# Kernel optimization log

Measured on AMD Instinct MI355X. Metric: run time of the kernel, lower is better.

## Reference

```python
import jax, jax.numpy as jnp
import numpy as np

B = 64            # batch
C = 2             # num_channels (BSF syndrome: X and Z)
L = 64            # lattice size
N = 16            # gradient (histogram) size
BIN = 360 // N    # bin_size = 22 degrees
EPS = 1e-5        # BatchNorm2d default eps


def setup_inputs() -> dict:
    key = jax.random.key(0)
    k1, = jax.random.split(key, 1)
    # syndrome in BSF: binary 0/1 values (torch.nonzero picks the set bits)
    x = jax.random.randint(k1, (B, C * L * L * L), 0, 2).astype(jnp.float32)
    gamma = jnp.ones((C,), jnp.float32)   # BatchNorm2d weight
    beta = jnp.zeros((C,), jnp.float32)   # BatchNorm2d bias
    return {"x": x, "gamma": gamma, "beta": beta}


def _bin_tables():
    # Per lattice site (i,j,k): magnitude and flattened (ax, az) bin index.
    c = jnp.arange(L, dtype=jnp.float32)
    i = c[:, None, None]
    j = c[None, :, None]
    k = c[None, None, :]
    mag = jnp.sqrt(i * i + j * j + k * k)          # (L,L,L)
    x_comp = jnp.sqrt(j * j + k * k)
    z_comp = jnp.sqrt(j * j + i * i)
    deg = 180.0 / jnp.pi
    # atan2 results are in [0, pi] here, so int() truncation == floor
    ax = jnp.floor(jnp.arctan2(x_comp, i) * deg / BIN).astype(jnp.int32)
    az = jnp.floor(jnp.arctan2(k, z_comp) * deg / BIN).astype(jnp.int32)
    bins = (ax * N + az).reshape(-1)               # (L^3,) flattened (ax,az)
    return mag.reshape(-1), bins


def reference(x, gamma, beta):
    mag, bins = _bin_tables()
    # torch.nonzero + indexed update == mask-weighted scatter of magnitudes.
    # x is 0/1, so x * mag equals the mags of the nonzero sites (0 elsewhere).
    xw = x.reshape(B, C, L * L * L) * mag                     # (B,C,L^3)
    g = jnp.zeros((B, C, N * N), x.dtype).at[:, :, bins].add(xw)
    g = g.reshape(B, C, N, N)
    # BatchNorm2d, training mode: per-channel batch statistics (biased var)
    mean = g.mean(axis=(0, 2, 3), keepdims=True)
    var = ((g - mean) ** 2).mean(axis=(0, 2, 3), keepdims=True)
    gn = (g - mean) * jax.lax.rsqrt(var + EPS)
    return gn * gamma[None, :, None, None] + beta[None, :, None, None]
```

## Files before the change

### kernel.cpp

```cpp
#include <hip/hip_runtime.h>


#define BINS_PAD 80
#define SLOTS 10

__global__ __launch_bounds__(256)
void bin_table_kernel(unsigned char* __restrict__ tab,
                      float* __restrict__ g,
                      float* __restrict__ mag) {
    int v = blockIdx.x * 256 + threadIdx.x;
    int i = v >> 12, j = (v >> 6) & 63, k = v & 63;
    double xc2 = (double)(j * j + k * k);
    double zc2 = (double)(i * i + j * j);
    double i2  = (double)(i * i);
    double k2  = (double)(k * k);
    const double T1 = 0.4040262258351568  * 0.4040262258351568;
    const double T2 = 0.9656887748070740  * 0.9656887748070740;
    const double T3 = 2.2460367739042161  * 2.2460367739042161;
    const double T4 = 28.636253282915602  * 28.636253282915602;
    int ax = (xc2 > i2 * T1) + (xc2 > i2 * T2) + (xc2 > i2 * T3) + (xc2 > i2 * T4);
    int az = (k2 > zc2 * T1) + (k2 > zc2 * T2) + (k2 > zc2 * T3) + (k2 > zc2 * T4);
    tab[v] = (unsigned char)(ax * 16 + az);
    float kf  = (float)k;
    float r2f = (float)(i * i + j * j);
    mag[v] = sqrtf(fmaf(kf, kf, r2f));
    if (v < 32768) g[v] = 0.0f;
}

__global__ __launch_bounds__(256)
void scatter_kernel(const float4* __restrict__ x4,
                    const uint4* __restrict__ tab4,
                    const float4* __restrict__ mag4,
                    float* __restrict__ g) {
    __shared__ unsigned long long slot[256][SLOTS];
    __shared__ float hist[BINS_PAD];
    int tid = threadIdx.x;
    int p   = blockIdx.x >> 6;
    int i   = blockIdx.x & 63;

    const unsigned long long SENT = ((unsigned long long)69u) << 32;
    #pragma unroll
    for (int s = 0; s < SLOTS; ++s) slot[tid][s] = SENT;
    if (tid < BINS_PAD) hist[tid] = 0.0f;

    const float4* xs = x4 + (size_t)p * 65536 + (size_t)i * 1024 + 4 * (size_t)tid;
    const float4* ms = mag4 + (size_t)i * 1024 + 4 * (size_t)tid;
    uint4  tb  = tab4[i * 256 + tid];
    float4 xq0 = xs[0], xq1 = xs[1], xq2 = xs[2], xq3 = xs[3];
    float4 mq0 = ms[0], mq1 = ms[1], mq2 = ms[2], mq3 = ms[3];

    float4       xq[4] = {xq0, xq1, xq2, xq3};
    float4       mq[4] = {mq0, mq1, mq2, mq3};
    unsigned int uq[4] = {tb.x, tb.y, tb.z, tb.w};

    int          prev = -1;
    unsigned int off  = (unsigned int)-8;
    float        acc  = 0.0f;
    char* myslot = (char*)slot[tid];

    #pragma unroll
    for (int q = 0; q < 4; ++q) {
        unsigned int u = uq[q];
        #pragma unroll
        for (int e = 0; e < 4; ++e) {
            float xe = (e == 0) ? xq[q].x : (e == 1) ? xq[q].y : (e == 2) ? xq[q].z : xq[q].w;
            float me = (e == 0) ? mq[q].x : (e == 1) ? mq[q].y : (e == 2) ? mq[q].z : mq[q].w;
            float val = xe * me;
            int   b   = (u >> (8 * e)) & 255;
            bool  ch  = (b != prev);
            off += ch ? 8u : 0u;
            acc  = ch ? val : (acc + val);
            prev = b;
            *(unsigned long long*)(myslot + off) =
                (((unsigned long long)(unsigned)b) << 32)
              | (unsigned long long)__float_as_uint(acc);
        }
    }
    __syncthreads();

    unsigned long long* mys = slot[tid];
    #pragma unroll
    for (int s = 0; s < SLOTS; ++s) {
        unsigned long long pk = mys[s];
        float av = __uint_as_float((unsigned int)pk);
        if (av != 0.0f) {
            unsigned int bb = (unsigned int)(pk >> 32);
            atomicAdd(&hist[bb], av);
        }
    }
    __syncthreads();

    if (tid < BINS_PAD) {
        float hv = hist[tid];
        if (hv != 0.0f) atomicAdd(&g[p * 256 + tid], hv);
    }
}

__global__ __launch_bounds__(1024)
void norm_kernel(const float4* __restrict__ g4,
                 const float* __restrict__ gamma,
                 const float* __restrict__ beta,
                 float4* __restrict__ out4) {
    __shared__ double red[16][4];
    __shared__ float  coef[4];
    int t = threadIdx.x;
    float4 vals[8];
    double s0 = 0.0, s1 = 0.0, q0 = 0.0, q1 = 0.0;
    #pragma unroll
    for (int n = 0; n < 8; ++n) {
        int idx = t + n * 1024;
        float4 v = g4[idx];
        vals[n] = v;
        double a = (double)v.x + (double)v.y + (double)v.z + (double)v.w;
        double b = (double)v.x * (double)v.x + (double)v.y * (double)v.y
                 + (double)v.z * (double)v.z + (double)v.w * (double)v.w;
        if ((idx >> 6) & 1) { s1 += a; q1 += b; }
        else                { s0 += a; q0 += b; }
    }
    #pragma unroll
    for (int offm = 32; offm > 0; offm >>= 1) {
        s0 += __shfl_down(s0, offm);
        s1 += __shfl_down(s1, offm);
        q0 += __shfl_down(q0, offm);
        q1 += __shfl_down(q1, offm);
    }
    int wave = t >> 6;
    if ((t & 63) == 0) {
        red[wave][0] = s0; red[wave][1] = s1; red[wave][2] = q0; red[wave][3] = q1;
    }
    __syncthreads();
    if (t == 0) {
        double S0 = 0, S1 = 0, Q0 = 0, Q1 = 0;
        for (int wv = 0; wv < 16; ++wv) {
            S0 += red[wv][0]; S1 += red[wv][1]; Q0 += red[wv][2]; Q1 += red[wv][3];
        }
        const double inv_n = 1.0 / 16384.0;
        double m0 = S0 * inv_n, m1 = S1 * inv_n;
        double v0 = Q0 * inv_n - m0 * m0;
        double v1 = Q1 * inv_n - m1 * m1;
        double r0 = 1.0 / sqrt(v0 + 1e-5);
        double r1 = 1.0 / sqrt(v1 + 1e-5);
        float g0 = gamma[0], g1 = gamma[1], b0 = beta[0], b1 = beta[1];
        coef[0] = (float)r0 * g0;
        coef[1] = (float)r1 * g1;
        coef[2] = b0 - (float)(m0 * r0) * g0;
        coef[3] = b1 - (float)(m1 * r1) * g1;
    }
    __syncthreads();
    float sc0 = coef[0], sc1 = coef[1], sh0 = coef[2], sh1 = coef[3];
    #pragma unroll
    for (int n = 0; n < 8; ++n) {
        int idx = t + n * 1024;
        int c = (idx >> 6) & 1;
        float sc = c ? sc1 : sc0;
        float sh = c ? sh1 : sh0;
        float4 v = vals[n];
        float4 o;
        o.x = v.x * sc + sh; o.y = v.y * sc + sh;
        o.z = v.z * sc + sh; o.w = v.w * sc + sh;
        out4[idx] = o;
    }
}

extern "C" void kernel_launch(void* const* d_in, const int* in_sizes, int n_in,
                              void* d_out, int out_size, void* d_ws, size_t ws_size,
                              hipStream_t stream) {
    const float* x     = (const float*)d_in[0];
    const float* gamma = (const float*)d_in[1];
    const float* beta  = (const float*)d_in[2];
    float* out = (float*)d_out;

    unsigned char* tab = (unsigned char*)d_ws;
    float*         g   = (float*)((char*)d_ws + 262144);
    float*         mag = (float*)((char*)d_ws + 393216);

    bin_table_kernel<<<1024, 256, 0, stream>>>(tab, g, mag);
    scatter_kernel<<<8192, 256, 0, stream>>>((const float4*)x, (const uint4*)tab,
                                             (const float4*)mag, g);
    norm_kernel<<<1, 1024, 0, stream>>>((const float4*)g, gamma, beta, (float4*)out);
}
```

Measured before the change: 197.6 us.

## Vectorize bin-table writes, transpose LDS slots, use nontemporal x loads

```diff
diff --git a/kernel.cpp b/kernel.cpp
--- a/kernel.cpp
+++ b/kernel.cpp
@@ -4,27 +4,47 @@
 #define BINS_PAD 80
 #define SLOTS 10
 
+typedef float fx4 __attribute__((ext_vector_type(4)));
+
 __global__ __launch_bounds__(256)
-void bin_table_kernel(unsigned char* __restrict__ tab,
-                      float* __restrict__ g,
-                      float* __restrict__ mag) {
-    int v = blockIdx.x * 256 + threadIdx.x;
-    int i = v >> 12, j = (v >> 6) & 63, k = v & 63;
-    double xc2 = (double)(j * j + k * k);
+void bin_table_kernel(uchar4* __restrict__ tab4,
+                      float4* __restrict__ g4,
+                      float4* __restrict__ mag4) {
+    int t4 = blockIdx.x * 256 + threadIdx.x;
+    int v0 = t4 << 2;
+    int i  = v0 >> 12;
+    int j  = (v0 >> 6) & 63;
+    int kb = v0 & 63;
+    double i2  = (double)(i * i);
     double zc2 = (double)(i * i + j * j);
-    double i2  = (double)(i * i);
-    double k2  = (double)(k * k);
     const double T1 = 0.4040262258351568  * 0.4040262258351568;
     const double T2 = 0.9656887748070740  * 0.9656887748070740;
     const double T3 = 2.2460367739042161  * 2.2460367739042161;
     const double T4 = 28.636253282915602  * 28.636253282915602;
-    int ax = (xc2 > i2 * T1) + (xc2 > i2 * T2) + (xc2 > i2 * T3) + (xc2 > i2 * T4);
-    int az = (k2 > zc2 * T1) + (k2 > zc2 * T2) + (k2 > zc2 * T3) + (k2 > zc2 * T4);
-    tab[v] = (unsigned char)(ax * 16 + az);
-    float kf  = (float)k;
+    double a1 = i2 * T1,  a2 = i2 * T2,  a3 = i2 * T3,  a4 = i2 * T4;
+    double z1 = zc2 * T1, z2 = zc2 * T2, z3 = zc2 * T3, z4 = zc2 * T4;
+    unsigned char tt[4];
+    float         mm[4];
     float r2f = (float)(i * i + j * j);
-    mag[v] = sqrtf(fmaf(kf, kf, r2f));
-    if (v < 32768) g[v] = 0.0f;
+    #pragma unroll
+    for (int e = 0; e < 4; ++e) {
+        int k = kb + e;
+        double xc2 = (double)(j * j + k * k);
+        double k2  = (double)(k * k);
+        int ax = (xc2 > a1) + (xc2 > a2) + (xc2 > a3) + (xc2 > a4);
+        int az = (k2 > z1) + (k2 > z2) + (k2 > z3) + (k2 > z4);
+        tt[e] = (unsigned char)(ax * 16 + az);
+        float kf = (float)k;
+        mm[e] = sqrtf(fmaf(kf, kf, r2f));
+    }
+    uchar4 tb; tb.x = tt[0]; tb.y = tt[1]; tb.z = tt[2]; tb.w = tt[3];
+    float4 mg; mg.x = mm[0]; mg.y = mm[1]; mg.z = mm[2]; mg.w = mm[3];
+    tab4[t4] = tb;
+    mag4[t4] = mg;
+    if (t4 < 8192) {
+        float4 z; z.x = 0.0f; z.y = 0.0f; z.z = 0.0f; z.w = 0.0f;
+        g4[t4] = z;
+    }
 }
 
 __global__ __launch_bounds__(256)
@@ -32,7 +52,7 @@
                     const uint4* __restrict__ tab4,
                     const float4* __restrict__ mag4,
                     float* __restrict__ g) {
-    __shared__ unsigned long long slot[256][SLOTS];
+    __shared__ unsigned long long slot[SLOTS][256];
     __shared__ float hist[BINS_PAD];
     int tid = threadIdx.x;
     int p   = blockIdx.x >> 6;
@@ -40,23 +60,30 @@
 
     const unsigned long long SENT = ((unsigned long long)69u) << 32;
     #pragma unroll
-    for (int s = 0; s < SLOTS; ++s) slot[tid][s] = SENT;
+    for (int s = 0; s < SLOTS; ++s) slot[s][tid] = SENT;
     if (tid < BINS_PAD) hist[tid] = 0.0f;
 
-    const float4* xs = x4 + (size_t)p * 65536 + (size_t)i * 1024 + 4 * (size_t)tid;
+    const fx4* xs = (const fx4*)x4 + (size_t)p * 65536 + (size_t)i * 1024 + 4 * (size_t)tid;
     const float4* ms = mag4 + (size_t)i * 1024 + 4 * (size_t)tid;
     uint4  tb  = tab4[i * 256 + tid];
-    float4 xq0 = xs[0], xq1 = xs[1], xq2 = xs[2], xq3 = xs[3];
+    fx4 nq0 = __builtin_nontemporal_load(xs + 0);
+    fx4 nq1 = __builtin_nontemporal_load(xs + 1);
+    fx4 nq2 = __builtin_nontemporal_load(xs + 2);
+    fx4 nq3 = __builtin_nontemporal_load(xs + 3);
     float4 mq0 = ms[0], mq1 = ms[1], mq2 = ms[2], mq3 = ms[3];
 
-    float4       xq[4] = {xq0, xq1, xq2, xq3};
+    float4 xq[4];
+    xq[0].x = nq0.x; xq[0].y = nq0.y; xq[0].z = nq0.z; xq[0].w = nq0.w;
+    xq[1].x = nq1.x; xq[1].y = nq1.y; xq[1].z = nq1.z; xq[1].w = nq1.w;
+    xq[2].x = nq2.x; xq[2].y = nq2.y; xq[2].z = nq2.z; xq[2].w = nq2.w;
+    xq[3].x = nq3.x; xq[3].y = nq3.y; xq[3].z = nq3.z; xq[3].w = nq3.w;
     float4       mq[4] = {mq0, mq1, mq2, mq3};
     unsigned int uq[4] = {tb.x, tb.y, tb.z, tb.w};
 
     int          prev = -1;
-    unsigned int off  = (unsigned int)-8;
+    unsigned int off  = (unsigned int)(tid * 8) - 2048u;
     float        acc  = 0.0f;
-    char* myslot = (char*)slot[tid];
+    char* base = (char*)slot;
 
     #pragma unroll
     for (int q = 0; q < 4; ++q) {
@@ -68,20 +95,19 @@
             float val = xe * me;
             int   b   = (u >> (8 * e)) & 255;
             bool  ch  = (b != prev);
-            off += ch ? 8u : 0u;
+            off += ch ? 2048u : 0u;
             acc  = ch ? val : (acc + val);
             prev = b;
-            *(unsigned long long*)(myslot + off) =
+            *(unsigned long long*)(base + off) =
                 (((unsigned long long)(unsigned)b) << 32)
               | (unsigned long long)__float_as_uint(acc);
         }
     }
     __syncthreads();
 
-    unsigned long long* mys = slot[tid];
     #pragma unroll
     for (int s = 0; s < SLOTS; ++s) {
-        unsigned long long pk = mys[s];
+        unsigned long long pk = slot[s][tid];
         float av = __uint_as_float((unsigned int)pk);
         if (av != 0.0f) {
             unsigned int bb = (unsigned int)(pk >> 32);
@@ -174,7 +200,7 @@
     float*         g   = (float*)((char*)d_ws + 262144);
     float*         mag = (float*)((char*)d_ws + 393216);
 
-    bin_table_kernel<<<1024, 256, 0, stream>>>(tab, g, mag);
+    bin_table_kernel<<<256, 256, 0, stream>>>((uchar4*)tab, (float4*)g, (float4*)mag);
     scatter_kernel<<<8192, 256, 0, stream>>>((const float4*)x, (const uint4*)tab,
                                              (const float4*)mag, g);
     norm_kernel<<<1, 1024, 0, stream>>>((const float4*)g, gamma, beta, (float4*)out);
```

Result: slower. 213.0 us (+7.8%).
